# Kernel optimization log

Hardware: AMD Instinct MI355X
Metric: run time of the kernel (lower is better)

The kernel has to match this reference:

```python
import jax, jax.numpy as jnp
import numpy as np

N_NODES = 100000
N_EDGES = 1200000
N_GRAPHS = 2048
VOCAB = 10000
D = 64
C = 2


def setup_inputs() -> dict:
    key = jax.random.key(0)
    ks = jax.random.split(key, 12)
    x = jax.random.randint(ks[0], (N_NODES,), 0, VOCAB)
    edge_index = jax.random.randint(ks[1], (2, N_EDGES), 0, N_NODES)
    batch = jnp.sort(jax.random.randint(ks[2], (N_NODES,), 0, N_GRAPHS))
    s = 0.1
    return {
        'x': x,
        'edge_index': edge_index,
        'batch': batch,
        'emb': jax.random.normal(ks[3], (VOCAB, D), jnp.float32) * s,
        'W1l': jax.random.normal(ks[4], (D, D), jnp.float32) * s,
        'b1l': jnp.zeros((D,), jnp.float32),
        'W1r': jax.random.normal(ks[5], (D, D), jnp.float32) * s,
        'W2l': jax.random.normal(ks[6], (D, D), jnp.float32) * s,
        'b2l': jnp.zeros((D,), jnp.float32),
        'W2r': jax.random.normal(ks[7], (D, D), jnp.float32) * s,
        'Wout': jax.random.normal(ks[8], (C, D), jnp.float32) * s,
        'bout': jnp.zeros((C,), jnp.float32),
    }


def _sage(h, src, dst, Wl, bl, Wr, n_nodes):
    # mean aggregation of source messages onto target nodes (PyG SAGEConv, aggr='mean')
    agg = jax.ops.segment_sum(h[src], dst, num_segments=n_nodes)  # [N, D]
    cnt = jax.ops.segment_sum(jnp.ones((src.shape[0],), h.dtype), dst, num_segments=n_nodes)
    agg = agg / jnp.maximum(cnt, 1.0)[:, None]
    # lin_l(agg) + lin_r(root); lin_l carries the bias, lin_r has none
    return agg @ Wl.T + bl + h @ Wr.T


def reference(x, edge_index, batch, emb, W1l, b1l, W1r, W2l, b2l, W2r, Wout, bout):
    src, dst = edge_index[0], edge_index[1]
    h = emb[x]                                   # [N, D] embedding lookup
    h = jax.nn.relu(_sage(h, src, dst, W1l, b1l, W1r, N_NODES))
    h = jax.nn.relu(_sage(h, src, dst, W2l, b2l, W2r, N_NODES))
    # global mean pool per graph
    pooled = jax.ops.segment_sum(h, batch, num_segments=N_GRAPHS)
    gcnt = jax.ops.segment_sum(jnp.ones((N_NODES,), h.dtype), batch, num_segments=N_GRAPHS)
    pooled = pooled / jnp.maximum(gcnt, 1.0)[:, None]
    return pooled @ Wout.T + bout                # [G, C]
```

## Files before the change

### kernel.cpp

```cpp
#include <hip/hip_runtime.h>

#define NN 100000
#define NE 1200000
#define NG 2048
#define VOCAB 10000
#define D 64
#define C 2

#define NBK 196
#define BSH 9
#define SLOT 7168

typedef _Float16 half8 __attribute__((ext_vector_type(8)));
typedef _Float16 half2 __attribute__((ext_vector_type(2)));

#if __has_builtin(__builtin_amdgcn_fdot2)
#define FDOT2(a, b, c) __builtin_amdgcn_fdot2((a), (b), (c), false)
#else
#define FDOT2(a, b, c) ((float)(a)[0] * (float)(b)[0] + (float)(a)[1] * (float)(b)[1] + (c))
#endif

__device__ __forceinline__ int atomAddI(int* p, int v) {
    return __hip_atomic_fetch_add(p, v, __ATOMIC_RELAXED, __HIP_MEMORY_SCOPE_AGENT);
}
__device__ __forceinline__ void atomAddF(float* p, float v) {
    __hip_atomic_fetch_add(p, v, __ATOMIC_RELAXED, __HIP_MEMORY_SCOPE_AGENT);
}

__global__ void __launch_bounds__(256) k_prep(const float4* __restrict__ emb4,
        half8* __restrict__ embh,
        const float* __restrict__ W1l, const float* __restrict__ W1r,
        const float* __restrict__ W2l, const float* __restrict__ W2r,
        half2* __restrict__ wp,
        const int* __restrict__ batch, int* __restrict__ gs) {
    int blk = blockIdx.x;
    if (blk < 313) {
        int i = blk * 256 + threadIdx.x;
        if (i >= VOCAB * 8) return;
        float4 a = emb4[(size_t)i * 2], b = emb4[(size_t)i * 2 + 1];
        half8 h;
        h[0] = (_Float16)a.x; h[1] = (_Float16)a.y; h[2] = (_Float16)a.z; h[3] = (_Float16)a.w;
        h[4] = (_Float16)b.x; h[5] = (_Float16)b.y; h[6] = (_Float16)b.z; h[7] = (_Float16)b.w;
        embh[i] = h;
    } else if (blk < 345) {
        int i = (blk - 313) * 256 + threadIdx.x;
        if (i >= 4 * 2048) return;
        int mat = i >> 11, idx = i & 2047;
        const float* W = (mat == 0) ? W1l : (mat == 1) ? W1r : (mat == 2) ? W2l : W2r;
        int row = idx >> 5, kk = idx & 31;
        half2 o;
        o[0] = (_Float16)W[row * 64 + 2 * kk];
        o[1] = (_Float16)W[row * 64 + 2 * kk + 1];
        wp[i] = o;
    } else {
        int n = (blk - 345) * 256 + threadIdx.x;
        if (n >= NN) return;
        int b = batch[n];
        if (n == 0) {
            for (int g = 0; g <= b; ++g) gs[g] = 0;
        } else {
            int bp = batch[n - 1];
            for (int g = bp + 1; g <= b; ++g) gs[g] = n;
        }
        if (n == NN - 1) {
            for (int g = b + 1; g <= NG; ++g) gs[g] = NN;
        }
    }
}

__global__ void __launch_bounds__(256) k_bucket(const int* __restrict__ src,
        const int* __restrict__ dst, int* __restrict__ bcur, unsigned* __restrict__ barr) {
    __shared__ int hcnt[NBK], hbase[NBK], hrank[NBK];
    int tid = threadIdx.x;
    if (tid < NBK) { hcnt[tid] = 0; hrank[tid] = 0; }
    __syncthreads();
    int per = (NE + gridDim.x - 1) / gridDim.x;
    int e0 = blockIdx.x * per, e1 = min(e0 + per, NE);
    for (int e = e0 + tid; e < e1; e += 256)
        atomicAdd(&hcnt[dst[e] >> BSH], 1);
    __syncthreads();
    if (tid < NBK) {
        int c = hcnt[tid];
        hbase[tid] = c ? atomAddI(&bcur[tid], c) : 0;
    }
    __syncthreads();
    for (int e = e0 + tid; e < e1; e += 256) {
        int d = dst[e], s = src[e];
        int b = d >> BSH;
        int r = atomicAdd(&hrank[b], 1);
        barr[(size_t)b * SLOT + hbase[b] + r] = ((unsigned)s << BSH) | (unsigned)(d & 511);
    }
}

__global__ void __launch_bounds__(256) k_bscan(const int* __restrict__ bcur,
        int* __restrict__ bstart, int* __restrict__ start) {
    __shared__ int sm[256];
    int t = threadIdx.x;
    int v0 = (t < NBK) ? bcur[t] : 0;
    sm[t] = v0;
    __syncthreads();
    for (int off = 1; off < 256; off <<= 1) {
        int v = (t >= off) ? sm[t - off] : 0;
        __syncthreads();
        sm[t] += v;
        __syncthreads();
    }
    if (t < NBK) bstart[t] = sm[t] - v0;
    if (t == 0) { bstart[NBK] = NE; start[NN] = NE; }
}

__global__ void __launch_bounds__(512) k_sortb(const int* __restrict__ bcur,
        const int* __restrict__ bstart, const unsigned* __restrict__ barr,
        const int* __restrict__ x,
        int* __restrict__ start, int* __restrict__ csr, unsigned short* __restrict__ xcsr) {
    __shared__ int cnt[512], loc[512], sm[512];
    int t = threadIdx.x;
    int b = blockIdx.x;
    cnt[t] = 0;
    __syncthreads();
    int count = bcur[b];
    int base  = bstart[b];
    const unsigned* bp = barr + (size_t)b * SLOT;
    for (int i = t; i < count; i += 512)
        atomicAdd(&cnt[bp[i] & 511], 1);
    __syncthreads();
    int own = cnt[t];
    sm[t] = own;
    __syncthreads();
    for (int off = 1; off < 512; off <<= 1) {
        int v = (t >= off) ? sm[t - off] : 0;
        __syncthreads();
        sm[t] += v;
        __syncthreads();
    }
    int ex = sm[t] - own;
    loc[t] = ex;
    int g0 = b << BSH;
    if (g0 + t < NN) start[g0 + t] = base + ex;
    __syncthreads();
    for (int i = t; i < count; i += 512) {
        unsigned p = bp[i];
        int r = atomicAdd(&loc[p & 511], 1);
        int sn = (int)(p >> BSH);
        csr[base + r]  = sn;
        xcsr[base + r] = (unsigned short)x[sn];
    }
}

__global__ void __launch_bounds__(256) k_agg1(const int* __restrict__ start,
        const unsigned short* __restrict__ idx, const half8* __restrict__ embh,
        half8* __restrict__ aggh) {
    int tid = threadIdx.x;
    int lane = tid & 63, wave = tid >> 6;
    int f = lane & 7;
    int nsub = lane >> 3;
    int n = blockIdx.x * 32 + wave * 8 + nsub;

    float pf = 0.f;
    {
        int i = blockIdx.x * 256 + tid;
        if (i < VOCAB * 8) { float4 v = ((const float4*)embh)[i]; pf = v.x; }
    }
    asm volatile("" : "+v"(pf));
    if (n >= NN) return;

    int s0 = start[n], s1 = start[n + 1];
    float inv = 1.0f / (float)max(s1 - s0, 1);
    float a[8] = {0.f, 0.f, 0.f, 0.f, 0.f, 0.f, 0.f, 0.f};
    int i = s0;
    for (; i + 4 <= s1; i += 4) {
        int c0 = idx[i], c1 = idx[i + 1], c2 = idx[i + 2], c3 = idx[i + 3];
        half8 v0 = embh[(size_t)c0 * 8 + f];
        half8 v1 = embh[(size_t)c1 * 8 + f];
        half8 v2 = embh[(size_t)c2 * 8 + f];
        half8 v3 = embh[(size_t)c3 * 8 + f];
#pragma unroll
        for (int k = 0; k < 8; ++k)
            a[k] += ((float)v0[k] + (float)v1[k]) + ((float)v2[k] + (float)v3[k]);
    }
    for (; i < s1; ++i) {
        half8 v = embh[(size_t)idx[i] * 8 + f];
#pragma unroll
        for (int k = 0; k < 8; ++k) a[k] += (float)v[k];
    }
    half8 o;
#pragma unroll
    for (int k = 0; k < 8; ++k) o[k] = (_Float16)(a[k] * inv);
    aggh[(size_t)f * NN + n] = o;
}

__global__ void __launch_bounds__(256) k_agg2h(const int* __restrict__ start,
        const int* __restrict__ idx, const half8* __restrict__ gsrc,
        half8* __restrict__ aggh) {
    int tid = threadIdx.x;
    int lane = tid & 63, wave = tid >> 6;
    int c     = blockIdx.x & 3;
    int half_ = (blockIdx.x >> 2) & 1;
    int nb    = blockIdx.x >> 3;
    int f4 = lane & 1, nsub = lane >> 1;
    const half8* gsl = gsrc + (size_t)c * NN * 2;

    float pf = 0.f;
    {
        int i = half_ * 100000 + nb * 256 + tid;
        if (i < NN * 2) { float4 v = ((const float4*)gsl)[i]; pf = v.x; }
    }
    asm volatile("" : "+v"(pf));

    int nloc = nb * 128 + wave * 32 + nsub;
    if (nloc >= NN / 2) return;
    int n = half_ * (NN / 2) + nloc;
    int s0 = start[n], s1 = start[n + 1];
    float inv = 1.0f / (float)max(s1 - s0, 1);
    float a[8] = {0.f, 0.f, 0.f, 0.f, 0.f, 0.f, 0.f, 0.f};
    int i = s0;
    for (; i + 4 <= s1; i += 4) {
        int c0 = idx[i], c1 = idx[i + 1], c2 = idx[i + 2], c3 = idx[i + 3];
        half8 v0 = gsl[(size_t)c0 * 2 + f4];
        half8 v1 = gsl[(size_t)c1 * 2 + f4];
        half8 v2 = gsl[(size_t)c2 * 2 + f4];
        half8 v3 = gsl[(size_t)c3 * 2 + f4];
#pragma unroll
        for (int k = 0; k < 8; ++k)
            a[k] += ((float)v0[k] + (float)v1[k]) + ((float)v2[k] + (float)v3[k]);
    }
    for (; i < s1; ++i) {
        half8 v = gsl[(size_t)idx[i] * 2 + f4];
#pragma unroll
        for (int k = 0; k < 8; ++k) a[k] += (float)v[k];
    }
    half8 o;
#pragma unroll
    for (int k = 0; k < 8; ++k) o[k] = (_Float16)(a[k] * inv);
    aggh[(size_t)(2 * c + f4) * NN + n] = o;
}

__global__ void __launch_bounds__(256) k_lin1(const half8* __restrict__ aggh,
        const int* __restrict__ x, const half8* __restrict__ embh,
        const half2* __restrict__ wl, const float* __restrict__ bl,
        const half2* __restrict__ wr, half8* __restrict__ outh) {
    int lane = threadIdx.x & 63;
    int h = __builtin_amdgcn_readfirstlane(threadIdx.x >> 6);
    int nn = blockIdx.x * 64 + lane;
    bool valid = nn < NN;
    int n = valid ? nn : NN - 1;

    float acc[16];
#pragma unroll
    for (int d = 0; d < 16; ++d) acc[d] = bl[h * 16 + d];

    const half8* ap = aggh + n;
    const half8* rp = embh + (size_t)x[n] * 8;
    const half2* wlH = wl + (size_t)h * 16 * 32;
    const half2* wrH = wr + (size_t)h * 16 * 32;

    half8 ah = ap[0];
    half8 rh = rp[0];
    for (int c = 0; c < 8; ++c) {
        half2 a2[4] = { __builtin_shufflevector(ah, ah, 0, 1),
                        __builtin_shufflevector(ah, ah, 2, 3),
                        __builtin_shufflevector(ah, ah, 4, 5),
                        __builtin_shufflevector(ah, ah, 6, 7) };
        half2 r2[4] = { __builtin_shufflevector(rh, rh, 0, 1),
                        __builtin_shufflevector(rh, rh, 2, 3),
                        __builtin_shufflevector(rh, rh, 4, 5),
                        __builtin_shufflevector(rh, rh, 6, 7) };
        if (c < 7) {
            ah = ap[(size_t)(c + 1) * NN];
            rh = rp[c + 1];
        }
        const half2* wlc = wlH + c * 4;
        const half2* wrc = wrH + c * 4;
#pragma unroll
        for (int d = 0; d < 16; ++d) {
#pragma unroll
            for (int kk = 0; kk < 4; ++kk) {
                acc[d] = FDOT2(a2[kk], wlc[d * 32 + kk], acc[d]);
                acc[d] = FDOT2(r2[kk], wrc[d * 32 + kk], acc[d]);
            }
        }
    }

    if (valid) {
        half8 o0, o1;
#pragma unroll
        for (int k = 0; k < 8; ++k) {
            o0[k] = (_Float16)fmaxf(acc[k], 0.f);
            o1[k] = (_Float16)fmaxf(acc[8 + k], 0.f);
        }
        half8* op = outh + ((size_t)h * NN + n) * 2;
        op[0] = o0; op[1] = o1;
    }
}

__global__ void __launch_bounds__(256) k_lin2p(const half8* __restrict__ aggh,
        const half8* __restrict__ rooth, const int* __restrict__ batch,
        const half2* __restrict__ wl, const float* __restrict__ bl,
        const half2* __restrict__ wr, float* __restrict__ pooled) {
    int lane = threadIdx.x & 63;
    int h = __builtin_amdgcn_readfirstlane(threadIdx.x >> 6);
    int nn = blockIdx.x * 64 + lane;
    bool valid = nn < NN;
    int n = valid ? nn : NN - 1;

    float acc[16];
#pragma unroll
    for (int d = 0; d < 16; ++d) acc[d] = bl[h * 16 + d];

    const half8* ap = aggh + n;
    const half8* rp = rooth + (size_t)n * 2;
    const size_t rcstep = (size_t)NN * 2;
    const half2* wlH = wl + (size_t)h * 16 * 32;
    const half2* wrH = wr + (size_t)h * 16 * 32;

    half8 ah = ap[0];
    half8 rh = rp[0];
    for (int c = 0; c < 8; ++c) {
        half2 a2[4] = { __builtin_shufflevector(ah, ah, 0, 1),
                        __builtin_shufflevector(ah, ah, 2, 3),
                        __builtin_shufflevector(ah, ah, 4, 5),
                        __builtin_shufflevector(ah, ah, 6, 7) };
        half2 r2[4] = { __builtin_shufflevector(rh, rh, 0, 1),
                        __builtin_shufflevector(rh, rh, 2, 3),
                        __builtin_shufflevector(rh, rh, 4, 5),
                        __builtin_shufflevector(rh, rh, 6, 7) };
        if (c < 7) {
            ah = ap[(size_t)(c + 1) * NN];
            int cn = c + 1;
            rh = rp[(size_t)(cn >> 1) * rcstep + (cn & 1)];
        }
        const half2* wlc = wlH + c * 4;
        const half2* wrc = wrH + c * 4;
#pragma unroll
        for (int d = 0; d < 16; ++d) {
#pragma unroll
            for (int kk = 0; kk < 4; ++kk) {
                acc[d] = FDOT2(a2[kk], wlc[d * 32 + kk], acc[d]);
                acc[d] = FDOT2(r2[kk], wrc[d * 32 + kk], acc[d]);
            }
        }
    }

    int g = batch[n];
    int g1  = __shfl_up(g, 1);
    int g2  = __shfl_up(g, 2);
    int g4  = __shfl_up(g, 4);
    int g8  = __shfl_up(g, 8);
    int g16 = __shfl_up(g, 16);
    int g32 = __shfl_up(g, 32);
    bool s1  = (lane >= 1)  && (g1 == g);
    bool s2  = (lane >= 2)  && (g2 == g);
    bool s4  = (lane >= 4)  && (g4 == g);
    bool s8  = (lane >= 8)  && (g8 == g);
    bool s16 = (lane >= 16) && (g16 == g);
    bool s32 = (lane >= 32) && (g32 == g);
    int gn = __shfl_down(g, 1);
    bool isLast = (lane == 63) || (gn != g);
    float* pg = pooled + (size_t)g * D + h * 16;
#pragma unroll
    for (int d = 0; d < 16; ++d) {
        float v = valid ? fmaxf(acc[d], 0.f) : 0.f;
        float t;
        t = __shfl_up(v, 1);  v += s1  ? t : 0.f;
        t = __shfl_up(v, 2);  v += s2  ? t : 0.f;
        t = __shfl_up(v, 4);  v += s4  ? t : 0.f;
        t = __shfl_up(v, 8);  v += s8  ? t : 0.f;
        t = __shfl_up(v, 16); v += s16 ? t : 0.f;
        t = __shfl_up(v, 32); v += s32 ? t : 0.f;
        if (isLast) atomAddF(pg + d, v);
    }
}

__global__ void __launch_bounds__(256) k_out(const int* __restrict__ gs,
        const float* __restrict__ pooled, const float* __restrict__ Wout,
        const float* __restrict__ bout, float* __restrict__ out) {
    int lane = threadIdx.x & 63;
    int wave = threadIdx.x >> 6;
    int g = blockIdx.x * 4 + wave;
    int s0 = gs[g], s1 = gs[g + 1];
    float p = pooled[(size_t)g * D + lane] / (float)max(s1 - s0, 1);
    float c0 = p * Wout[lane];
    float c1 = p * Wout[D + lane];
#pragma unroll
    for (int off = 32; off > 0; off >>= 1) {
        c0 += __shfl_down(c0, off, 64);
        c1 += __shfl_down(c1, off, 64);
    }
    if (lane == 0) {
        out[g * C + 0] = c0 + bout[0];
        out[g * C + 1] = c1 + bout[1];
    }
}

extern "C" void kernel_launch(void* const* d_in, const int* in_sizes, int n_in,
                              void* d_out, int out_size, void* d_ws, size_t ws_size,
                              hipStream_t stream) {
    const int*   x     = (const int*)d_in[0];
    const int*   src   = (const int*)d_in[1];
    const int*   dst   = src + NE;
    const int*   batch = (const int*)d_in[2];
    const float* emb   = (const float*)d_in[3];
    const float* W1l   = (const float*)d_in[4];
    const float* b1l   = (const float*)d_in[5];
    const float* W1r   = (const float*)d_in[6];
    const float* W2l   = (const float*)d_in[7];
    const float* b2l   = (const float*)d_in[8];
    const float* W2r   = (const float*)d_in[9];
    const float* Wout  = (const float*)d_in[10];
    const float* bout  = (const float*)d_in[11];
    float* out = (float*)d_out;

    _Float16* TAh  = (_Float16*)d_ws;
    _Float16* T0h  = TAh + (size_t)NN * 64;
    _Float16* embh = T0h + (size_t)NN * 64;
    _Float16* wpck = embh + (size_t)VOCAB * 64;
    float* pooled  = (float*)(wpck + 16384);
    int* bcur   = (int*)(pooled + (size_t)NG * 64);
    int* bstart = bcur + NBK;
    int* startA = bstart + NBK + 1;
    int* gs     = startA + NN + 1;
    int* csr    = gs + NG + 1;
    unsigned short* xcsr = (unsigned short*)(csr + NE);
    unsigned* barr = (unsigned*)(xcsr + NE);
    half2* wp = (half2*)wpck;

    hipMemsetAsync(pooled, 0, ((size_t)NG * 64 + NBK) * sizeof(float), stream);

    k_prep  <<<736, 256, 0, stream>>>((const float4*)emb, (half8*)embh,
                                      W1l, W1r, W2l, W2r, wp, batch, gs);
    k_bucket<<<384, 256, 0, stream>>>(src, dst, bcur, barr);
    k_bscan <<<1, 256, 0, stream>>>(bcur, bstart, startA);
    k_sortb <<<NBK, 512, 0, stream>>>(bcur, bstart, barr, x, startA, csr, xcsr);

    int linGrid = (NN + 63) / 64;
    k_agg1<<<NN / 32, 256, 0, stream>>>(startA, xcsr, (const half8*)embh, (half8*)TAh);
    k_lin1<<<linGrid, 256, 0, stream>>>((const half8*)TAh, x, (const half8*)embh,
                                        wp, b1l, wp + 2048, (half8*)T0h);
    k_agg2h<<<((NN / 2 + 127) / 128) * 8, 256, 0, stream>>>(startA, csr, (const half8*)T0h, (half8*)TAh);
    k_lin2p<<<linGrid, 256, 0, stream>>>((const half8*)TAh, (const half8*)T0h, batch,
                                         wp + 4096, b2l, wp + 6144, pooled);

    k_out<<<NG / 4, 256, 0, stream>>>(gs, pooled, Wout, bout, out);
}
```

Before: 227.3 us.

## Fuse neighbor aggregation into linear layers via shared-memory staging

Merges each SAGE layer's gather/mean aggregation kernel with its linear+ReLU kernel. The aggregated 64-wide rows for 64 nodes are staged in XOR-swizzled LDS instead of a global intermediate buffer, which removes two kernel launches and a full N×64 write-and-read round trip. The layer-1 output layout also changes from feature-chunk-major to node-major, so the layer-2 gather reads one contiguous 128-byte row per neighbor instead of using the previous channel-split blocking. The cost is that the gather phase loses the previous layer-2 L2-locality partitioning and each block now serializes gather, barrier and matmul.

```diff
diff --git a/kernel.cpp b/kernel.cpp
--- a/kernel.cpp
+++ b/kernel.cpp
@@ -147,100 +147,56 @@
     }
 }
 
-__global__ void __launch_bounds__(256) k_agg1(const int* __restrict__ start,
+__global__ void __launch_bounds__(256) k_l1(const int* __restrict__ start,
         const unsigned short* __restrict__ idx, const half8* __restrict__ embh,
-        half8* __restrict__ aggh) {
+        const int* __restrict__ x,
+        const half2* __restrict__ wl, const float* __restrict__ bl,
+        const half2* __restrict__ wr, half8* __restrict__ h1) {
+    __shared__ half8 smA[64][8];
     int tid = threadIdx.x;
     int lane = tid & 63, wave = tid >> 6;
-    int f = lane & 7;
-    int nsub = lane >> 3;
-    int n = blockIdx.x * 32 + wave * 8 + nsub;
 
     float pf = 0.f;
     {
         int i = blockIdx.x * 256 + tid;
-        if (i < VOCAB * 8) { float4 v = ((const float4*)embh)[i]; pf = v.x; }
+        if (i < VOCAB * 8) { float4 v = ((const float4*)embh)[i]; pf = v.x * 0.f; }
     }
     asm volatile("" : "+v"(pf));
-    if (n >= NN) return;
-
-    int s0 = start[n], s1 = start[n + 1];
-    float inv = 1.0f / (float)max(s1 - s0, 1);
-    float a[8] = {0.f, 0.f, 0.f, 0.f, 0.f, 0.f, 0.f, 0.f};
-    int i = s0;
-    for (; i + 4 <= s1; i += 4) {
-        int c0 = idx[i], c1 = idx[i + 1], c2 = idx[i + 2], c3 = idx[i + 3];
-        half8 v0 = embh[(size_t)c0 * 8 + f];
-        half8 v1 = embh[(size_t)c1 * 8 + f];
-        half8 v2 = embh[(size_t)c2 * 8 + f];
-        half8 v3 = embh[(size_t)c3 * 8 + f];
-#pragma unroll
-        for (int k = 0; k < 8; ++k)
-            a[k] += ((float)v0[k] + (float)v1[k]) + ((float)v2[k] + (float)v3[k]);
-    }
-    for (; i < s1; ++i) {
-        half8 v = embh[(size_t)idx[i] * 8 + f];
-#pragma unroll
-        for (int k = 0; k < 8; ++k) a[k] += (float)v[k];
-    }
-    half8 o;
-#pragma unroll
-    for (int k = 0; k < 8; ++k) o[k] = (_Float16)(a[k] * inv);
-    aggh[(size_t)f * NN + n] = o;
-}
-
-__global__ void __launch_bounds__(256) k_agg2h(const int* __restrict__ start,
-        const int* __restrict__ idx, const half8* __restrict__ gsrc,
-        half8* __restrict__ aggh) {
-    int tid = threadIdx.x;
-    int lane = tid & 63, wave = tid >> 6;
-    int c     = blockIdx.x & 3;
-    int half_ = (blockIdx.x >> 2) & 1;
-    int nb    = blockIdx.x >> 3;
-    int f4 = lane & 1, nsub = lane >> 1;
-    const half8* gsl = gsrc + (size_t)c * NN * 2;
-
-    float pf = 0.f;
-    {
-        int i = half_ * 100000 + nb * 256 + tid;
-        if (i < NN * 2) { float4 v = ((const float4*)gsl)[i]; pf = v.x; }
-    }
-    asm volatile("" : "+v"(pf));
-
-    int nloc = nb * 128 + wave * 32 + nsub;
-    if (nloc >= NN / 2) return;
-    int n = half_ * (NN / 2) + nloc;
-    int s0 = start[n], s1 = start[n + 1];
-    float inv = 1.0f / (float)max(s1 - s0, 1);
-    float a[8] = {0.f, 0.f, 0.f, 0.f, 0.f, 0.f, 0.f, 0.f};
-    int i = s0;
-    for (; i + 4 <= s1; i += 4) {
-        int c0 = idx[i], c1 = idx[i + 1], c2 = idx[i + 2], c3 = idx[i + 3];
-        half8 v0 = gsl[(size_t)c0 * 2 + f4];
-        half8 v1 = gsl[(size_t)c1 * 2 + f4];
-        half8 v2 = gsl[(size_t)c2 * 2 + f4];
-        half8 v3 = gsl[(size_t)c3 * 2 + f4];
-#pragma unroll
-        for (int k = 0; k < 8; ++k)
-            a[k] += ((float)v0[k] + (float)v1[k]) + ((float)v2[k] + (float)v3[k]);
-    }
-    for (; i < s1; ++i) {
-        half8 v = gsl[(size_t)idx[i] * 2 + f4];
-#pragma unroll
-        for (int k = 0; k < 8; ++k) a[k] += (float)v[k];
-    }
-    half8 o;
-#pragma unroll
-    for (int k = 0; k < 8; ++k) o[k] = (_Float16)(a[k] * inv);
-    aggh[(size_t)(2 * c + f4) * NN + n] = o;
-}
-
-__global__ void __launch_bounds__(256) k_lin1(const half8* __restrict__ aggh,
-        const int* __restrict__ x, const half8* __restrict__ embh,
-        const half2* __restrict__ wl, const float* __restrict__ bl,
-        const half2* __restrict__ wr, half8* __restrict__ outh) {
-    int lane = threadIdx.x & 63;
-    int h = __builtin_amdgcn_readfirstlane(threadIdx.x >> 6);
+
+    int f = lane & 7;
+#pragma unroll
+    for (int r = 0; r < 2; ++r) {
+        int nl = r * 32 + wave * 8 + (lane >> 3);
+        int n = blockIdx.x * 64 + nl;
+        if (n < NN) {
+            int s0 = start[n], s1 = start[n + 1];
+            float inv = 1.0f / (float)max(s1 - s0, 1);
+            float a[8] = {pf, 0.f, 0.f, 0.f, 0.f, 0.f, 0.f, 0.f};
+            int i = s0;
+            for (; i + 4 <= s1; i += 4) {
+                int c0 = idx[i], c1 = idx[i + 1], c2 = idx[i + 2], c3 = idx[i + 3];
+                half8 v0 = embh[(size_t)c0 * 8 + f];
+                half8 v1 = embh[(size_t)c1 * 8 + f];
+                half8 v2 = embh[(size_t)c2 * 8 + f];
+                half8 v3 = embh[(size_t)c3 * 8 + f];
+#pragma unroll
+                for (int k = 0; k < 8; ++k)
+                    a[k] += ((float)v0[k] + (float)v1[k]) + ((float)v2[k] + (float)v3[k]);
+            }
+            for (; i < s1; ++i) {
+                half8 v = embh[(size_t)idx[i] * 8 + f];
+#pragma unroll
+                for (int k = 0; k < 8; ++k) a[k] += (float)v[k];
+            }
+            half8 o;
+#pragma unroll
+            for (int k = 0; k < 8; ++k) o[k] = (_Float16)(a[k] * inv);
+            smA[nl][f ^ (nl & 7)] = o;
+        }
+    }
+    __syncthreads();
+
+    int h = __builtin_amdgcn_readfirstlane(wave);
     int nn = blockIdx.x * 64 + lane;
     bool valid = nn < NN;
     int n = valid ? nn : NN - 1;
@@ -248,13 +204,11 @@
     float acc[16];
 #pragma unroll
     for (int d = 0; d < 16; ++d) acc[d] = bl[h * 16 + d];
-
-    const half8* ap = aggh + n;
     const half8* rp = embh + (size_t)x[n] * 8;
     const half2* wlH = wl + (size_t)h * 16 * 32;
     const half2* wrH = wr + (size_t)h * 16 * 32;
 
-    half8 ah = ap[0];
+    half8 ah = smA[lane][0 ^ (lane & 7)];
     half8 rh = rp[0];
     for (int c = 0; c < 8; ++c) {
         half2 a2[4] = { __builtin_shufflevector(ah, ah, 0, 1),
@@ -266,7 +220,7 @@
                         __builtin_shufflevector(rh, rh, 4, 5),
                         __builtin_shufflevector(rh, rh, 6, 7) };
         if (c < 7) {
-            ah = ap[(size_t)(c + 1) * NN];
+            ah = smA[lane][(c + 1) ^ (lane & 7)];
             rh = rp[c + 1];
         }
         const half2* wlc = wlH + c * 4;
@@ -288,17 +242,54 @@
             o0[k] = (_Float16)fmaxf(acc[k], 0.f);
             o1[k] = (_Float16)fmaxf(acc[8 + k], 0.f);
         }
-        half8* op = outh + ((size_t)h * NN + n) * 2;
-        op[0] = o0; op[1] = o1;
-    }
-}
-
-__global__ void __launch_bounds__(256) k_lin2p(const half8* __restrict__ aggh,
-        const half8* __restrict__ rooth, const int* __restrict__ batch,
+        h1[(size_t)n * 8 + 2 * h]     = o0;
+        h1[(size_t)n * 8 + 2 * h + 1] = o1;
+    }
+}
+
+__global__ void __launch_bounds__(256) k_l2(const int* __restrict__ start,
+        const int* __restrict__ idx, const half8* __restrict__ h1,
+        const int* __restrict__ batch,
         const half2* __restrict__ wl, const float* __restrict__ bl,
         const half2* __restrict__ wr, float* __restrict__ pooled) {
-    int lane = threadIdx.x & 63;
-    int h = __builtin_amdgcn_readfirstlane(threadIdx.x >> 6);
+    __shared__ half8 smA[64][8];
+    int tid = threadIdx.x;
+    int lane = tid & 63, wave = tid >> 6;
+
+    int f = lane & 7;
+#pragma unroll
+    for (int r = 0; r < 2; ++r) {
+        int nl = r * 32 + wave * 8 + (lane >> 3);
+        int n = blockIdx.x * 64 + nl;
+        if (n < NN) {
+            int s0 = start[n], s1 = start[n + 1];
+            float inv = 1.0f / (float)max(s1 - s0, 1);
+            float a[8] = {0.f, 0.f, 0.f, 0.f, 0.f, 0.f, 0.f, 0.f};
+            int i = s0;
+            for (; i + 4 <= s1; i += 4) {
+                int c0 = idx[i], c1 = idx[i + 1], c2 = idx[i + 2], c3 = idx[i + 3];
+                half8 v0 = h1[(size_t)c0 * 8 + f];
+                half8 v1 = h1[(size_t)c1 * 8 + f];
+                half8 v2 = h1[(size_t)c2 * 8 + f];
+                half8 v3 = h1[(size_t)c3 * 8 + f];
+#pragma unroll
+                for (int k = 0; k < 8; ++k)
+                    a[k] += ((float)v0[k] + (float)v1[k]) + ((float)v2[k] + (float)v3[k]);
+            }
+            for (; i < s1; ++i) {
+                half8 v = h1[(size_t)idx[i] * 8 + f];
+#pragma unroll
+                for (int k = 0; k < 8; ++k) a[k] += (float)v[k];
+            }
+            half8 o;
+#pragma unroll
+            for (int k = 0; k < 8; ++k) o[k] = (_Float16)(a[k] * inv);
+            smA[nl][f ^ (nl & 7)] = o;
+        }
+    }
+    __syncthreads();
+
+    int h = __builtin_amdgcn_readfirstlane(wave);
     int nn = blockIdx.x * 64 + lane;
     bool valid = nn < NN;
     int n = valid ? nn : NN - 1;
@@ -306,14 +297,11 @@
     float acc[16];
 #pragma unroll
     for (int d = 0; d < 16; ++d) acc[d] = bl[h * 16 + d];
-
-    const half8* ap = aggh + n;
-    const half8* rp = rooth + (size_t)n * 2;
-    const size_t rcstep = (size_t)NN * 2;
+    const half8* rp = h1 + (size_t)n * 8;
     const half2* wlH = wl + (size_t)h * 16 * 32;
     const half2* wrH = wr + (size_t)h * 16 * 32;
 
-    half8 ah = ap[0];
+    half8 ah = smA[lane][0 ^ (lane & 7)];
     half8 rh = rp[0];
     for (int c = 0; c < 8; ++c) {
         half2 a2[4] = { __builtin_shufflevector(ah, ah, 0, 1),
@@ -325,9 +313,8 @@
                         __builtin_shufflevector(rh, rh, 4, 5),
                         __builtin_shufflevector(rh, rh, 6, 7) };
         if (c < 7) {
-            ah = ap[(size_t)(c + 1) * NN];
-            int cn = c + 1;
-            rh = rp[(size_t)(cn >> 1) * rcstep + (cn & 1)];
+            ah = smA[lane][(c + 1) ^ (lane & 7)];
+            rh = rp[c + 1];
         }
         const half2* wlc = wlH + c * 4;
         const half2* wrc = wrH + c * 4;
@@ -410,8 +397,7 @@
     const float* bout  = (const float*)d_in[11];
     float* out = (float*)d_out;
 
-    _Float16* TAh  = (_Float16*)d_ws;
-    _Float16* T0h  = TAh + (size_t)NN * 64;
+    _Float16* T0h  = (_Float16*)d_ws;
     _Float16* embh = T0h + (size_t)NN * 64;
     _Float16* wpck = embh + (size_t)VOCAB * 64;
     float* pooled  = (float*)(wpck + 16384);
@@ -432,13 +418,11 @@
     k_bscan <<<1, 256, 0, stream>>>(bcur, bstart, startA);
     k_sortb <<<NBK, 512, 0, stream>>>(bcur, bstart, barr, x, startA, csr, xcsr);
 
-    int linGrid = (NN + 63) / 64;
-    k_agg1<<<NN / 32, 256, 0, stream>>>(startA, xcsr, (const half8*)embh, (half8*)TAh);
-    k_lin1<<<linGrid, 256, 0, stream>>>((const half8*)TAh, x, (const half8*)embh,
+    int fusedGrid = (NN + 63) / 64;
+    k_l1<<<fusedGrid, 256, 0, stream>>>(startA, xcsr, (const half8*)embh, x,
                                         wp, b1l, wp + 2048, (half8*)T0h);
-    k_agg2h<<<((NN / 2 + 127) / 128) * 8, 256, 0, stream>>>(startA, csr, (const half8*)T0h, (half8*)TAh);
-    k_lin2p<<<linGrid, 256, 0, stream>>>((const half8*)TAh, (const half8*)T0h, batch,
-                                         wp + 4096, b2l, wp + 6144, pooled);
+    k_l2<<<fusedGrid, 256, 0, stream>>>(startA, csr, (const half8*)T0h, batch,
+                                        wp + 4096, b2l, wp + 6144, pooled);
 
     k_out<<<NG / 4, 256, 0, stream>>>(gs, pooled, Wout, bout, out);
 }
```

New measurement: 206.5 us. 1.1x faster.
